# Optimization experiments

Hardware: AMD Instinct MI355X
Metric: run time of the kernel (lower is better)

Reference implementation:

```python
import jax, jax.numpy as jnp
import numpy as np
from jax import lax

# Model dims (match init_kwargs / input_specs)
B, T, N_IN, N_MID, N_OUT = 256, 100, 784, 1024, 10
L_TAU = 0.8  # state decay


def setup_inputs() -> dict:
    key = jax.random.key(0)
    ks = jax.random.split(key, 10)
    x = jax.random.uniform(ks[0], (B, T, N_IN), dtype=jnp.float32)  # input spikes/rates
    y = jax.random.randint(ks[1], (B,), 0, N_OUT, dtype=jnp.int64)

    def lin(k, fan_in, fan_out):
        return jax.random.normal(k, (fan_in, fan_out), dtype=jnp.float32) / np.sqrt(fan_in)

    return {
        "x": x, "y": y,
        "W1": lin(ks[2], N_IN, N_MID),  "b1": jnp.zeros((N_MID,), jnp.float32),
        "W2": lin(ks[3], N_MID, N_MID), "b2": jnp.zeros((N_MID,), jnp.float32),
        "W3": lin(ks[4], N_MID, N_MID), "b3": jnp.zeros((N_MID,), jnp.float32),
        "W4": lin(ks[5], N_MID, N_OUT), "b4": jnp.zeros((N_OUT,), jnp.float32),
    }


def _snu(s, y_prev, x_in, W, b):
    # SNU cell (soft): s_t = relu(W x_t + tau * s_{t-1} * (1 - y_{t-1})); y_t = sigmoid(s_t + b)
    s = jax.nn.relu(x_in @ W + L_TAU * s * (1.0 - y_prev))
    y_out = jax.nn.sigmoid(s + b)
    return s, y_out


def reference(x, y, W1, b1, W2, b2, W3, b3, W4, b4):
    bsz = x.shape[0]
    zeros = lambda n: jnp.zeros((bsz, n), x.dtype)
    carry0 = (zeros(N_MID), zeros(N_MID), zeros(N_MID), zeros(N_MID),
              zeros(N_MID), zeros(N_MID), zeros(N_OUT), zeros(N_OUT))

    def step(carry, x_t):
        s1, y1, s2, y2, s3, y3, s4, y4 = carry
        s1, y1 = _snu(s1, y1, x_t, W1, b1)
        s2, y2 = _snu(s2, y2, y1, W2, b2)
        s3, y3 = _snu(s3, y3, y2, W3, b3)
        s4, y4 = _snu(s4, y4, y3, W4, b4)
        return (s1, y1, s2, y2, s3, y3, s4, y4), y4

    xs = jnp.transpose(x, (1, 0, 2))  # [T, B, n_in]
    _, outs = lax.scan(step, carry0, xs)  # outs: [T, B, n_out]
    # out_rec also stacked the initial zero output; it contributes 0 to the sum
    m = jnp.sum(outs, axis=0)  # [B, n_out]
    logp = jax.nn.log_softmax(m, axis=-1)
    loss = -jnp.mean(jnp.take_along_axis(logp, y[:, None], axis=1))
    return loss, m
```

## Files before the change

### kernel.cpp

```cpp
#include <hip/hip_runtime.h>
#include <hip/hip_bf16.h>


#define BDIM 256
#define TT   100
#define TP   112
#define BB   256
#define MM2  (BB * TP)
#define NMID 1024
#define K1   784
#define K1P  896
#define NOUT 10
#define N4P  16
#define L_TAU 0.8f

#define NBLK 256
#define ZST  102

typedef __attribute__((ext_vector_type(4))) int   int4x;
typedef __attribute__((ext_vector_type(8))) int   int8x;
typedef __attribute__((ext_vector_type(4))) float f32x4;

__device__ __forceinline__ void async_copy16(const void* g, void* l) {
    __builtin_amdgcn_global_load_lds(
        (const __attribute__((address_space(1))) unsigned int*)g,
        (__attribute__((address_space(3))) unsigned int*)l,
        16, 0, 0);
}

__device__ __forceinline__ unsigned short f2bf(float f) {
    __hip_bfloat16 h = __float2bfloat16(f);
    return __builtin_bit_cast(unsigned short, h);
}
__device__ __forceinline__ float bf2f(unsigned short u) {
    return __uint_as_float((unsigned)u << 16);
}

__global__ void convert_x(const float* __restrict__ X, unsigned char* __restrict__ XB) {
    int bid = blockIdx.x;
    int b = bid >> 2;
    int q = bid & 3;
    int th = threadIdx.x;
    if (th >= K1P / 4) return;
    const float4* xs = (const float4*)(X + ((long)b * TT + q * 25) * K1);
    unsigned char* xd = XB + ((long)b * TP + q * 25) * K1P;
    for (int tt = 0; tt < 25; ++tt) {
        int pk = 0;
        if (th < K1 / 4) {
            float4 v = xs[(long)tt * (K1 / 4) + th];
            pk = __builtin_amdgcn_cvt_pk_fp8_f32(v.x, v.y, 0, false);
            pk = __builtin_amdgcn_cvt_pk_fp8_f32(v.z, v.w, pk, true);
        }
        *(int*)(xd + (long)tt * K1P + th * 4) = pk;
    }
}

__device__ __forceinline__ void tc_body(const float* __restrict__ W,
                                        unsigned char* __restrict__ WT,
                                        int K, int N, int Kpad,
                                        int bx, int by, int tidx) {
    __shared__ float tile[32][33];
    int k0 = bx * 32;
    int n0 = by * 32;
    int tx = tidx & 31, ty = tidx >> 5;
    #pragma unroll
    for (int i = 0; i < 4; ++i) {
        int k = k0 + ty + i * 8;
        tile[ty + i * 8][tx] = (k < K) ? W[(long)k * N + n0 + tx] : 0.0f;
    }
    __syncthreads();
    int nl = tidx >> 3, kq = tidx & 7;
    int pk = __builtin_amdgcn_cvt_pk_fp8_f32(tile[kq * 4 + 0][nl], tile[kq * 4 + 1][nl], 0, false);
    pk     = __builtin_amdgcn_cvt_pk_fp8_f32(tile[kq * 4 + 2][nl], tile[kq * 4 + 3][nl], pk, true);
    *(int*)(WT + (long)(n0 + nl) * Kpad + k0 + kq * 4) = pk;
}

__global__ void transpose_convert(const float* __restrict__ W, unsigned char* __restrict__ WT,
                                  int K, int N, int Kpad) {
    tc_body(W, WT, K, N, Kpad, blockIdx.x, blockIdx.y, threadIdx.x);
}

__global__ void transpose_convert2(const float* __restrict__ Wa, unsigned char* __restrict__ Ta,
                                   const float* __restrict__ Wb, unsigned char* __restrict__ Tb) {
    const float* W = blockIdx.z ? Wb : Wa;
    unsigned char* T = blockIdx.z ? Tb : Ta;
    tc_body(W, T, NMID, NMID, NMID, blockIdx.x, blockIdx.y, threadIdx.x);
}

__global__ void convert_w4(const float* __restrict__ W4, unsigned char* __restrict__ W4T) {
    int tid = blockIdx.x * BDIM + threadIdx.x;
    int n = tid >> 8;
    int k4 = (tid & 255) * 4;
    float v0 = 0, v1 = 0, v2 = 0, v3 = 0;
    if (n < NOUT) {
        v0 = W4[(k4 + 0) * NOUT + n];
        v1 = W4[(k4 + 1) * NOUT + n];
        v2 = W4[(k4 + 2) * NOUT + n];
        v3 = W4[(k4 + 3) * NOUT + n];
    }
    int pk = __builtin_amdgcn_cvt_pk_fp8_f32(v0, v1, 0, false);
    pk     = __builtin_amdgcn_cvt_pk_fp8_f32(v2, v3, pk, true);
    *(int*)(W4T + (long)n * NMID + k4) = pk;
}

__device__ __forceinline__ void stage_tile(const unsigned char* Aptr,
                                           const unsigned char* Bptr,
                                           unsigned char* As, unsigned char* Bs,
                                           int srow, int lch, int Kp, int k0) {
    #pragma unroll
    for (int i = 0; i < 4; ++i)
        if (srow + i * 32 < TP)
            async_copy16(Aptr + (long)(i * 32) * Kp + k0,
                         &As[(srow + i * 32) * 128 + lch * 16]);
    #pragma unroll
    for (int i = 0; i < 8; ++i)
        async_copy16(Bptr + (long)(i * 32) * Kp + k0,
                     &Bs[(srow + i * 32) * 128 + lch * 16]);
}

__global__ __launch_bounds__(256, 3) void gemm_snu_fused(
    const unsigned char* __restrict__ A,
    const unsigned char* __restrict__ BT,
    const float* __restrict__ bias,
    unsigned char* __restrict__ Y,
    int Kp)
{
    __shared__ unsigned char smem[52224];
    unsigned char* As = smem;
    unsigned char* Bs = smem + 14336;
    unsigned short* Zs = (unsigned short*)smem;

    const int tid  = threadIdx.x;
    const int wave = tid >> 6;
    const int lane = tid & 63;

    const int l   = blockIdx.x;
    const int xcd = l & 7;
    const int p   = l >> 3;
    const int b   = xcd * 32 + (p >> 2);
    const int bn  = (p & 3) * NBLK;

    const long arow0 = (long)b * TP;

    const float bv = bias[bn + tid];
    unsigned char* yp = Y + arow0 * NMID + bn + tid;

    f32x4 acc[7][4] = {};

    const int srow = tid >> 3;
    const int lch  = tid & 7;
    const int gch  = lch ^ (srow & 7);
    const unsigned char* Aptr = A  + (arow0 + srow) * Kp + gch * 16;
    const unsigned char* Bptr = BT + (long)(bn + srow) * Kp + gch * 16;

    const int mrow = lane & 15;
    const int g    = lane >> 4;
    const int wc   = wave * 64;

    for (int k0 = 0; k0 < Kp; k0 += 128) {
        stage_tile(Aptr, Bptr, As, Bs, srow, lch, Kp, k0);
        __syncthreads();

        int8x bfr[4];
        #pragma unroll
        for (int j = 0; j < 4; ++j) {
            int row = wc + j * 16 + mrow;
            int r7  = row & 7;
            int4x lo = *(const int4x*)&Bs[row * 128 + ((2 * g    ) ^ r7) * 16];
            int4x hi = *(const int4x*)&Bs[row * 128 + ((2 * g + 1) ^ r7) * 16];
            bfr[j][0] = lo[0]; bfr[j][1] = lo[1]; bfr[j][2] = lo[2]; bfr[j][3] = lo[3];
            bfr[j][4] = hi[0]; bfr[j][5] = hi[1]; bfr[j][6] = hi[2]; bfr[j][7] = hi[3];
        }
        #pragma unroll
        for (int i = 0; i < 7; ++i) {
            int row = i * 16 + mrow;
            int r7  = row & 7;
            int4x lo = *(const int4x*)&As[row * 128 + ((2 * g    ) ^ r7) * 16];
            int4x hi = *(const int4x*)&As[row * 128 + ((2 * g + 1) ^ r7) * 16];
            int8x af;
            af[0] = lo[0]; af[1] = lo[1]; af[2] = lo[2]; af[3] = lo[3];
            af[4] = hi[0]; af[5] = hi[1]; af[6] = hi[2]; af[7] = hi[3];
            #pragma unroll
            for (int j = 0; j < 4; ++j)
                acc[i][j] = __builtin_amdgcn_mfma_scale_f32_16x16x128_f8f6f4(
                    bfr[j], af, acc[i][j],
                    0, 0,
                    0, 0x7F,
                    0, 0x7F);
        }
        __syncthreads();
    }

    #pragma unroll
    for (int i = 0; i < 7; ++i)
        #pragma unroll
        for (int j = 0; j < 4; ++j) {
            int t  = i * 16 + mrow;
            int nn = wc + j * 16 + g * 4;
            if (t < TT)
                #pragma unroll
                for (int r = 0; r < 4; ++r)
                    Zs[(nn + r) * ZST + t] = f2bf(acc[i][j][r]);
        }
    __syncthreads();

    {
        const unsigned short* zp = Zs + tid * ZST;
        float s = 0.0f, u = 1.0f;
        unsigned int zc = *(const unsigned int*)(zp);
        unsigned int z1 = *(const unsigned int*)(zp + 2);
        for (int t0 = 0; t0 < TT; t0 += 2) {
            unsigned int z2 = 0;
            if (t0 + 4 < TT) z2 = *(const unsigned int*)(zp + t0 + 4);
            float z = bf2f((unsigned short)(zc & 0xFFFFu));
            s = fmaxf(fmaf(L_TAU * s, u, z), 0.0f);
            u = __builtin_amdgcn_rcpf(1.0f + __expf(s + bv));
            yp[(long)t0 * NMID] = (unsigned char)(__builtin_amdgcn_cvt_pk_fp8_f32(1.0f - u, 0.0f, 0, false) & 0xFF);
            z = bf2f((unsigned short)(zc >> 16));
            s = fmaxf(fmaf(L_TAU * s, u, z), 0.0f);
            u = __builtin_amdgcn_rcpf(1.0f + __expf(s + bv));
            yp[(long)(t0 + 1) * NMID] = (unsigned char)(__builtin_amdgcn_cvt_pk_fp8_f32(1.0f - u, 0.0f, 0, false) & 0xFF);
            zc = z1; z1 = z2;
        }
    }
}

__global__ __launch_bounds__(256) void layer4_gemm(const unsigned char* __restrict__ Y3,
                                                   const unsigned char* __restrict__ W4T,
                                                   float* __restrict__ Z4) {
    const int tid  = threadIdx.x;
    const int wave = tid >> 6;
    const int lane = tid & 63;
    const int mrow = lane & 15;
    const int g    = lane >> 4;
    const int row  = blockIdx.x * 64 + wave * 16 + mrow;
    const unsigned char* ap = Y3  + (long)row  * NMID + g * 32;
    const unsigned char* wp = W4T + (long)mrow * NMID + g * 32;
    f32x4 acc = {};
    #pragma unroll
    for (int kt = 0; kt < 8; ++kt) {
        int4x alo = *(const int4x*)(ap + kt * 128);
        int4x ahi = *(const int4x*)(ap + kt * 128 + 16);
        int4x wlo = *(const int4x*)(wp + kt * 128);
        int4x whi = *(const int4x*)(wp + kt * 128 + 16);
        int8x af, bf;
        af[0] = alo[0]; af[1] = alo[1]; af[2] = alo[2]; af[3] = alo[3];
        af[4] = ahi[0]; af[5] = ahi[1]; af[6] = ahi[2]; af[7] = ahi[3];
        bf[0] = wlo[0]; bf[1] = wlo[1]; bf[2] = wlo[2]; bf[3] = wlo[3];
        bf[4] = whi[0]; bf[5] = whi[1]; bf[6] = whi[2]; bf[7] = whi[3];
        acc = __builtin_amdgcn_mfma_scale_f32_16x16x128_f8f6f4(
            bf, af, acc, 0, 0, 0, 0x7F, 0, 0x7F);
    }
    int bq = row / TP;
    int tq = row - bq * TP;
    float* zb = Z4 + ((long)bq * N4P + g * 4) * TP + tq;
    zb[0 * TP] = acc[0];
    zb[1 * TP] = acc[1];
    zb[2 * TP] = acc[2];
    zb[3 * TP] = acc[3];
}

__global__ void snu4_recur(const float* __restrict__ Z4, const float* __restrict__ b4,
                           float* __restrict__ m_out) {
    int idx = blockIdx.x * 64 + threadIdx.x;
    int n = idx & 15;
    int b = idx >> 4;
    if (n >= NOUT) return;
    float bv = b4[n];
    float s = 0.0f, u = 1.0f, msum = 0.0f;
    const float* zp = Z4 + ((long)b * N4P + n) * TP;
    for (int t0 = 0; t0 < TT; t0 += 4) {
        float4 zz = *(const float4*)(zp + t0);
        float z[4] = {zz.x, zz.y, zz.z, zz.w};
        #pragma unroll
        for (int j = 0; j < 4; ++j) {
            s = fmaxf(fmaf(L_TAU * s, u, z[j]), 0.0f);
            float e = __expf(s + bv);
            u = __builtin_amdgcn_rcpf(1.0f + e);
            msum += 1.0f - u;
        }
    }
    m_out[b * NOUT + n] = msum;
}

__global__ void loss_kernel(const float* __restrict__ m, const int* __restrict__ y,
                            float* __restrict__ out) {
    __shared__ float red[BDIM];
    int b = threadIdx.x;
    float v[NOUT];
    float mx = -1e30f;
    #pragma unroll
    for (int n = 0; n < NOUT; ++n) { v[n] = m[b * NOUT + n]; mx = fmaxf(mx, v[n]); }
    float se = 0.0f;
    #pragma unroll
    for (int n = 0; n < NOUT; ++n) se += __expf(v[n] - mx);
    float lse = mx + __logf(se);
    int lbl = y[b];
    float vy = 0.0f;
    #pragma unroll
    for (int n = 0; n < NOUT; ++n) if (n == lbl) vy = v[n];
    red[b] = -(vy - lse);
    __syncthreads();
    for (int off = 128; off; off >>= 1) {
        if (b < off) red[b] += red[b + off];
        __syncthreads();
    }
    if (b == 0) out[0] = red[0] / (float)BB;
}

extern "C" void kernel_launch(void* const* d_in, const int* in_sizes, int n_in,
                              void* d_out, int out_size, void* d_ws, size_t ws_size,
                              hipStream_t stream) {
    const float* x  = (const float*)d_in[0];
    const int*   y  = (const int*)  d_in[1];
    const float* W1 = (const float*)d_in[2];
    const float* b1 = (const float*)d_in[3];
    const float* W2 = (const float*)d_in[4];
    const float* b2 = (const float*)d_in[5];
    const float* W3 = (const float*)d_in[6];
    const float* b3 = (const float*)d_in[7];
    const float* W4 = (const float*)d_in[8];
    const float* b4 = (const float*)d_in[9];
    float* out = (float*)d_out;

    char* ws = (char*)d_ws;
    size_t off = 0;
    auto alloc = [&](size_t bytes) {
        char* p = ws + off;
        off = (off + bytes + 255) & ~(size_t)255;
        return (void*)p;
    };
    unsigned char* XB  = (unsigned char*)alloc((size_t)MM2 * K1P);
    unsigned char* W1T = (unsigned char*)alloc((size_t)NMID * K1P);
    unsigned char* W2T = (unsigned char*)alloc((size_t)NMID * NMID);
    unsigned char* W3T = (unsigned char*)alloc((size_t)NMID * NMID);
    unsigned char* W4T = (unsigned char*)alloc((size_t)N4P * NMID);
    unsigned char* Ya  = (unsigned char*)alloc((size_t)MM2 * NMID);
    unsigned char* Yb  = (unsigned char*)alloc((size_t)MM2 * NMID);
    float*         Z4  = (float*)        alloc((size_t)MM2 * N4P * 4);

    convert_x<<<BB * 4, BDIM, 0, stream>>>(x, XB);
    transpose_convert<<<dim3(K1P / 32, NMID / 32), BDIM, 0, stream>>>(W1, W1T, K1, NMID, K1P);
    transpose_convert2<<<dim3(NMID / 32, NMID / 32, 2), BDIM, 0, stream>>>(W2, W2T, W3, W3T);
    convert_w4<<<N4P * NMID / 4 / BDIM, BDIM, 0, stream>>>(W4, W4T);

    const int fblocks = BB * (NMID / NBLK);
    gemm_snu_fused<<<fblocks, BDIM, 0, stream>>>(XB, W1T, b1, Ya, K1P);
    gemm_snu_fused<<<fblocks, BDIM, 0, stream>>>(Ya, W2T, b2, Yb, NMID);
    gemm_snu_fused<<<fblocks, BDIM, 0, stream>>>(Yb, W3T, b3, Ya, NMID);
    layer4_gemm<<<MM2 / 64, BDIM, 0, stream>>>(Ya, W4T, Z4);
    snu4_recur<<<64, 64, 0, stream>>>(Z4, b4, out + 1);
    loss_kernel<<<1, BDIM, 0, stream>>>(out + 1, y, out);
}
```

Baseline: 346.5 us.

## Fuse weight/input prep kernels and merge layer-4 GEMM with output recurrence

Combines the input conversion and the three weight transpose/convert kernels into a single launch, dispatching by block index ranges. Fuses the layer-4 MFMA GEMM with the SNU output recurrence, one block per batch, so logits stay in LDS instead of passing through a global Z4 buffer. This removes three launches and a global round trip. The recurrence now runs on only 10 threads per block, and those blocks are serial chains.

```diff
diff --git a/kernel.cpp b/kernel.cpp
--- a/kernel.cpp
+++ b/kernel.cpp
@@ -17,6 +17,11 @@
 #define NBLK 256
 #define ZST  102
 
+#define PB_CX   1024
+#define PB_TC1  (PB_CX + 896)
+#define PB_TC23 (PB_TC1 + 2048)
+#define PB_W4   (PB_TC23 + 16)
+
 typedef __attribute__((ext_vector_type(4))) int   int4x;
 typedef __attribute__((ext_vector_type(8))) int   int8x;
 typedef __attribute__((ext_vector_type(4))) float f32x4;
@@ -34,25 +39,6 @@
 }
 __device__ __forceinline__ float bf2f(unsigned short u) {
     return __uint_as_float((unsigned)u << 16);
-}
-
-__global__ void convert_x(const float* __restrict__ X, unsigned char* __restrict__ XB) {
-    int bid = blockIdx.x;
-    int b = bid >> 2;
-    int q = bid & 3;
-    int th = threadIdx.x;
-    if (th >= K1P / 4) return;
-    const float4* xs = (const float4*)(X + ((long)b * TT + q * 25) * K1);
-    unsigned char* xd = XB + ((long)b * TP + q * 25) * K1P;
-    for (int tt = 0; tt < 25; ++tt) {
-        int pk = 0;
-        if (th < K1 / 4) {
-            float4 v = xs[(long)tt * (K1 / 4) + th];
-            pk = __builtin_amdgcn_cvt_pk_fp8_f32(v.x, v.y, 0, false);
-            pk = __builtin_amdgcn_cvt_pk_fp8_f32(v.z, v.w, pk, true);
-        }
-        *(int*)(xd + (long)tt * K1P + th * 4) = pk;
-    }
 }
 
 __device__ __forceinline__ void tc_body(const float* __restrict__ W,
@@ -75,32 +61,56 @@
     *(int*)(WT + (long)(n0 + nl) * Kpad + k0 + kq * 4) = pk;
 }
 
-__global__ void transpose_convert(const float* __restrict__ W, unsigned char* __restrict__ WT,
-                                  int K, int N, int Kpad) {
-    tc_body(W, WT, K, N, Kpad, blockIdx.x, blockIdx.y, threadIdx.x);
-}
-
-__global__ void transpose_convert2(const float* __restrict__ Wa, unsigned char* __restrict__ Ta,
-                                   const float* __restrict__ Wb, unsigned char* __restrict__ Tb) {
-    const float* W = blockIdx.z ? Wb : Wa;
-    unsigned char* T = blockIdx.z ? Tb : Ta;
-    tc_body(W, T, NMID, NMID, NMID, blockIdx.x, blockIdx.y, threadIdx.x);
-}
-
-__global__ void convert_w4(const float* __restrict__ W4, unsigned char* __restrict__ W4T) {
-    int tid = blockIdx.x * BDIM + threadIdx.x;
-    int n = tid >> 8;
-    int k4 = (tid & 255) * 4;
-    float v0 = 0, v1 = 0, v2 = 0, v3 = 0;
-    if (n < NOUT) {
-        v0 = W4[(k4 + 0) * NOUT + n];
-        v1 = W4[(k4 + 1) * NOUT + n];
-        v2 = W4[(k4 + 2) * NOUT + n];
-        v3 = W4[(k4 + 3) * NOUT + n];
-    }
-    int pk = __builtin_amdgcn_cvt_pk_fp8_f32(v0, v1, 0, false);
-    pk     = __builtin_amdgcn_cvt_pk_fp8_f32(v2, v3, pk, true);
-    *(int*)(W4T + (long)n * NMID + k4) = pk;
+__global__ __launch_bounds__(256) void prep_fused(
+    const float* __restrict__ X,  unsigned char* __restrict__ XB,
+    const float* __restrict__ W1, unsigned char* __restrict__ W1T,
+    const float* __restrict__ W2, unsigned char* __restrict__ W2T,
+    const float* __restrict__ W3, unsigned char* __restrict__ W3T,
+    const float* __restrict__ W4, unsigned char* __restrict__ W4T)
+{
+    const int bid = blockIdx.x;
+    const int th  = threadIdx.x;
+
+    if (bid < PB_CX) {
+        int b = bid >> 2;
+        int q = bid & 3;
+        if (th >= K1P / 4) return;
+        const float4* xs = (const float4*)(X + ((long)b * TT + q * 25) * K1);
+        unsigned char* xd = XB + ((long)b * TP + q * 25) * K1P;
+        for (int tt = 0; tt < 25; ++tt) {
+            int pk = 0;
+            if (th < K1 / 4) {
+                float4 v = xs[(long)tt * (K1 / 4) + th];
+                pk = __builtin_amdgcn_cvt_pk_fp8_f32(v.x, v.y, 0, false);
+                pk = __builtin_amdgcn_cvt_pk_fp8_f32(v.z, v.w, pk, true);
+            }
+            *(int*)(xd + (long)tt * K1P + th * 4) = pk;
+        }
+    } else if (bid < PB_TC1) {
+        int idx = bid - PB_CX;
+        tc_body(W1, W1T, K1, NMID, K1P, idx % 28, idx / 28, th);
+    } else if (bid < PB_TC23) {
+        int idx = bid - PB_TC1;
+        int z   = idx >> 10;
+        int rem = idx & 1023;
+        tc_body(z ? W3 : W2, z ? W3T : W2T, NMID, NMID, NMID,
+                rem & 31, rem >> 5, th);
+    } else {
+        int idx = bid - PB_TC23;
+        int tid = idx * BDIM + th;
+        int n = tid >> 8;
+        int k4 = (tid & 255) * 4;
+        float v0 = 0, v1 = 0, v2 = 0, v3 = 0;
+        if (n < NOUT) {
+            v0 = W4[(k4 + 0) * NOUT + n];
+            v1 = W4[(k4 + 1) * NOUT + n];
+            v2 = W4[(k4 + 2) * NOUT + n];
+            v3 = W4[(k4 + 3) * NOUT + n];
+        }
+        int pk = __builtin_amdgcn_cvt_pk_fp8_f32(v0, v1, 0, false);
+        pk     = __builtin_amdgcn_cvt_pk_fp8_f32(v2, v3, pk, true);
+        *(int*)(W4T + (long)n * NMID + k4) = pk;
+    }
 }
 
 __device__ __forceinline__ void stage_tile(const unsigned char* Aptr,
@@ -225,62 +235,65 @@
     }
 }
 
-__global__ __launch_bounds__(256) void layer4_gemm(const unsigned char* __restrict__ Y3,
-                                                   const unsigned char* __restrict__ W4T,
-                                                   float* __restrict__ Z4) {
+__global__ __launch_bounds__(256) void layer4_fused(
+    const unsigned char* __restrict__ Y3,
+    const unsigned char* __restrict__ W4T,
+    const float* __restrict__ b4,
+    float* __restrict__ m_out)
+{
+    __shared__ float Z4s[TP][N4P];
+
     const int tid  = threadIdx.x;
     const int wave = tid >> 6;
     const int lane = tid & 63;
     const int mrow = lane & 15;
     const int g    = lane >> 4;
-    const int row  = blockIdx.x * 64 + wave * 16 + mrow;
-    const unsigned char* ap = Y3  + (long)row  * NMID + g * 32;
-    const unsigned char* wp = W4T + (long)mrow * NMID + g * 32;
-    f32x4 acc = {};
-    #pragma unroll
-    for (int kt = 0; kt < 8; ++kt) {
-        int4x alo = *(const int4x*)(ap + kt * 128);
-        int4x ahi = *(const int4x*)(ap + kt * 128 + 16);
-        int4x wlo = *(const int4x*)(wp + kt * 128);
-        int4x whi = *(const int4x*)(wp + kt * 128 + 16);
-        int8x af, bf;
-        af[0] = alo[0]; af[1] = alo[1]; af[2] = alo[2]; af[3] = alo[3];
-        af[4] = ahi[0]; af[5] = ahi[1]; af[6] = ahi[2]; af[7] = ahi[3];
-        bf[0] = wlo[0]; bf[1] = wlo[1]; bf[2] = wlo[2]; bf[3] = wlo[3];
-        bf[4] = whi[0]; bf[5] = whi[1]; bf[6] = whi[2]; bf[7] = whi[3];
-        acc = __builtin_amdgcn_mfma_scale_f32_16x16x128_f8f6f4(
-            bf, af, acc, 0, 0, 0, 0x7F, 0, 0x7F);
-    }
-    int bq = row / TP;
-    int tq = row - bq * TP;
-    float* zb = Z4 + ((long)bq * N4P + g * 4) * TP + tq;
-    zb[0 * TP] = acc[0];
-    zb[1 * TP] = acc[1];
-    zb[2 * TP] = acc[2];
-    zb[3 * TP] = acc[3];
-}
-
-__global__ void snu4_recur(const float* __restrict__ Z4, const float* __restrict__ b4,
-                           float* __restrict__ m_out) {
-    int idx = blockIdx.x * 64 + threadIdx.x;
-    int n = idx & 15;
-    int b = idx >> 4;
-    if (n >= NOUT) return;
-    float bv = b4[n];
-    float s = 0.0f, u = 1.0f, msum = 0.0f;
-    const float* zp = Z4 + ((long)b * N4P + n) * TP;
-    for (int t0 = 0; t0 < TT; t0 += 4) {
-        float4 zz = *(const float4*)(zp + t0);
-        float z[4] = {zz.x, zz.y, zz.z, zz.w};
-        #pragma unroll
-        for (int j = 0; j < 4; ++j) {
-            s = fmaxf(fmaf(L_TAU * s, u, z[j]), 0.0f);
-            float e = __expf(s + bv);
-            u = __builtin_amdgcn_rcpf(1.0f + e);
+    const int b    = blockIdx.x;
+
+    int8x wf[8];
+    {
+        const unsigned char* wp = W4T + (long)mrow * NMID + g * 32;
+        #pragma unroll
+        for (int kt = 0; kt < 8; ++kt) {
+            int4x wlo = *(const int4x*)(wp + kt * 128);
+            int4x whi = *(const int4x*)(wp + kt * 128 + 16);
+            wf[kt][0] = wlo[0]; wf[kt][1] = wlo[1]; wf[kt][2] = wlo[2]; wf[kt][3] = wlo[3];
+            wf[kt][4] = whi[0]; wf[kt][5] = whi[1]; wf[kt][6] = whi[2]; wf[kt][7] = whi[3];
+        }
+    }
+
+    for (int rg = wave; rg < 7; rg += 4) {
+        const long row = (long)b * TP + rg * 16 + mrow;
+        const unsigned char* ap = Y3 + row * NMID + g * 32;
+        f32x4 acc = {};
+        #pragma unroll
+        for (int kt = 0; kt < 8; ++kt) {
+            int4x alo = *(const int4x*)(ap + kt * 128);
+            int4x ahi = *(const int4x*)(ap + kt * 128 + 16);
+            int8x af;
+            af[0] = alo[0]; af[1] = alo[1]; af[2] = alo[2]; af[3] = alo[3];
+            af[4] = ahi[0]; af[5] = ahi[1]; af[6] = ahi[2]; af[7] = ahi[3];
+            acc = __builtin_amdgcn_mfma_scale_f32_16x16x128_f8f6f4(
+                wf[kt], af, acc, 0, 0, 0, 0x7F, 0, 0x7F);
+        }
+        *(f32x4*)&Z4s[rg * 16 + mrow][g * 4] = acc;
+    }
+    __syncthreads();
+
+    if (tid < NOUT) {
+        const float bv = b4[tid];
+        float s = 0.0f, u = 1.0f, msum = 0.0f;
+        float zc = Z4s[0][tid];
+        float z1 = Z4s[1][tid];
+        for (int t = 0; t < TT; ++t) {
+            float z2 = (t + 2 < TT) ? Z4s[t + 2][tid] : 0.0f;
+            s = fmaxf(fmaf(L_TAU * s, u, zc), 0.0f);
+            u = __builtin_amdgcn_rcpf(1.0f + __expf(s + bv));
             msum += 1.0f - u;
-        }
-    }
-    m_out[b * NOUT + n] = msum;
+            zc = z1; z1 = z2;
+        }
+        m_out[b * NOUT + tid] = msum;
+    }
 }
 
 __global__ void loss_kernel(const float* __restrict__ m, const int* __restrict__ y,
@@ -337,18 +350,13 @@
     unsigned char* W4T = (unsigned char*)alloc((size_t)N4P * NMID);
     unsigned char* Ya  = (unsigned char*)alloc((size_t)MM2 * NMID);
     unsigned char* Yb  = (unsigned char*)alloc((size_t)MM2 * NMID);
-    float*         Z4  = (float*)        alloc((size_t)MM2 * N4P * 4);
-
-    convert_x<<<BB * 4, BDIM, 0, stream>>>(x, XB);
-    transpose_convert<<<dim3(K1P / 32, NMID / 32), BDIM, 0, stream>>>(W1, W1T, K1, NMID, K1P);
-    transpose_convert2<<<dim3(NMID / 32, NMID / 32, 2), BDIM, 0, stream>>>(W2, W2T, W3, W3T);
-    convert_w4<<<N4P * NMID / 4 / BDIM, BDIM, 0, stream>>>(W4, W4T);
+
+    prep_fused<<<PB_W4, BDIM, 0, stream>>>(x, XB, W1, W1T, W2, W2T, W3, W3T, W4, W4T);
 
     const int fblocks = BB * (NMID / NBLK);
     gemm_snu_fused<<<fblocks, BDIM, 0, stream>>>(XB, W1T, b1, Ya, K1P);
     gemm_snu_fused<<<fblocks, BDIM, 0, stream>>>(Ya, W2T, b2, Yb, NMID);
     gemm_snu_fused<<<fblocks, BDIM, 0, stream>>>(Yb, W3T, b3, Ya, NMID);
-    layer4_gemm<<<MM2 / 64, BDIM, 0, stream>>>(Ya, W4T, Z4);
-    snu4_recur<<<64, 64, 0, stream>>>(Z4, b4, out + 1);
+    layer4_fused<<<BB, BDIM, 0, stream>>>(Ya, W4T, b4, out + 1);
     loss_kernel<<<1, BDIM, 0, stream>>>(out + 1, y, out);
 }
```

Result: faster. 333.3 us (-3.8%).
